# Kernel optimization log

Hardware: AMD Instinct MI355X
Metric: run time of the kernel (lower is better)

Reference implementation:

```python
import jax, jax.numpy as jnp
import numpy as np

N = 50000
E = 800000
D_IN = 64
D_OUT = 64
H = 8
R = 8  # num_relations; relation id R is reserved for self-loops
NEG_SLOPE = 0.2
EPS = 1e-10


def setup_inputs() -> dict:
    key = jax.random.key(0)
    ks = jax.random.split(key, 7)
    x = jax.random.normal(ks[0], (N, D_IN), jnp.float32)
    # xavier_uniform-like scale for W_tau, kaiming-like for query
    w_scale = (6.0 / (D_IN + D_OUT)) ** 0.5
    W_tau = jax.random.normal(ks[1], (R + 1, D_OUT, D_IN), jnp.float32) * w_scale
    query = jax.random.normal(ks[2], (R + 1, H, 2 * D_OUT // H), jnp.float32) * 0.1
    node_in = jax.random.randint(ks[3], (E,), 0, N, jnp.int32)
    node_out = jax.random.randint(ks[4], (E,), 0, N, jnp.int32)
    relation = jax.random.randint(ks[5], (E,), 0, R, jnp.int32)
    edge_weight = jax.random.uniform(ks[6], (E,), jnp.float32)
    return {"x": x, "W_tau": W_tau, "query": query, "node_in": node_in,
            "node_out": node_out, "relation": relation, "edge_weight": edge_weight}


def reference(x, W_tau, query, node_in, node_out, relation, edge_weight):
    n_node = x.shape[0]
    rp1, d_out, _ = W_tau.shape  # num_relations + 1
    n_head = query.shape[1]

    # append self-loop edges with relation id = num_relations, weight 1
    self_idx = jnp.arange(n_node, dtype=node_in.dtype)
    ni = jnp.concatenate([node_in, self_idx])            # [M]
    no = jnp.concatenate([node_out, self_idx])           # [M]
    rel = jnp.concatenate([relation, jnp.full((n_node,), rp1 - 1, dtype=relation.dtype)])
    ew = jnp.concatenate([edge_weight, jnp.ones((n_node,), edge_weight.dtype)])[:, None]  # [M,1]

    # per-relation linear transform of all nodes: [R+1, N, D_out]
    hidden = jnp.einsum('rdi,ni->rnd', W_tau, x)

    # gather endpoint features per edge (relation-specific)
    h_in = hidden[rel, ni]    # [M, D_out]
    h_out = hidden[rel, no]   # [M, D_out]
    m = h_in.shape[0]

    # interleaved stack then head split, matching torch stack(dim=-1).view
    key_feat = jnp.stack([h_in, h_out], axis=-1).reshape(m, n_head, -1)  # [M,H,2*D/H]
    w = jnp.einsum('mhd,mhd->mh', query[rel], key_feat)                  # [M,H]
    w = jax.nn.leaky_relu(w, NEG_SLOPE)

    # segment softmax (stabilized by per-node max), normalizer is scatter-MEAN (faithful)
    mx = jax.ops.segment_max(w, no, num_segments=n_node)[no]
    att = jnp.exp(w - mx) * ew                                           # [M,H]
    cnt = jax.ops.segment_sum(jnp.ones((m,), x.dtype), no, num_segments=n_node)  # [N]
    norm = (jax.ops.segment_sum(att, no, num_segments=n_node) / cnt[:, None])[no]
    att = att / (norm + EPS)

    value = h_in.reshape(m, n_head, d_out // n_head)                     # [M,H,D/H]
    msg = (att[..., None] * value).reshape(m, d_out)                     # [M,D_out]

    # aggregate: scatter-mean over destination nodes, then ReLU (combine)
    update = jax.ops.segment_sum(msg, no, num_segments=n_node) / cnt[:, None]
    return jax.nn.relu(update)
```

## Files before the change

kernel.cpp:

```cpp
#include <hip/hip_runtime.h>
#include <math.h>

#define N_NODES 50000
#define N_EDGES 800000
#define DOUT 64
#define NHEAD 8
#define RP1 9
#define NEG_SLOPE 0.2f
#define EPS_F 1e-10f
#define M_TOT (N_EDGES + N_NODES)
#define NW (RP1 * DOUT * DOUT)
#define RNG (N_NODES / 8)
#define EPB 2048
#define CHUNKS ((M_TOT + EPB - 1) / EPB)
#define BUCK 48
#define MBLK ((M_TOT + 255) / 256)
#define FILLB (CHUNKS * 8)
#define K1B ((N_NODES + 63) / 64)
#define K1PAD 784

typedef __attribute__((ext_vector_type(8))) short bf16x8;
typedef __attribute__((ext_vector_type(4))) float f32x4;

__device__ __forceinline__ unsigned short f2bf(float f) {
    unsigned int u = __float_as_uint(f);
    unsigned int r = (u + 0x7FFFu + ((u >> 16) & 1u)) >> 16;
    return (unsigned short)r;
}
__device__ __forceinline__ float bf2f(unsigned short s) {
    return __uint_as_float(((unsigned int)s) << 16);
}

__global__ __launch_bounds__(256) void kprep2(const int* __restrict__ node_in,
                                              const int* __restrict__ relation,
                                              const float* __restrict__ edge_weight,
                                              const float* __restrict__ W,
                                              int2* __restrict__ meta_by_m,
                                              unsigned short* __restrict__ Wb,
                                              int* __restrict__ cursor) {
    int m = blockIdx.x * 256 + threadIdx.x;
    if (m < NW / 4) {
        int i = m * 4;
        float4 v = *(const float4*)(W + i);
        ushort4 o; o.x = f2bf(v.x); o.y = f2bf(v.y); o.z = f2bf(v.z); o.w = f2bf(v.w);
        *(ushort4*)(Wb + i) = o;
    }
    if (m < N_NODES) cursor[m] = 0;
    if (m >= M_TOT) return;
    int ni, rl; float ew;
    if (m < N_EDGES) {
        ni = node_in[m]; rl = relation[m]; ew = edge_weight[m];
    } else {
        ni = m - N_EDGES; rl = RP1 - 1; ew = 1.0f;
    }
    int2 v; v.x = ni | (rl << 16); v.y = __float_as_int(ew);
    meta_by_m[m] = v;
}

__global__ __launch_bounds__(256) void kbig(const float* __restrict__ x,
                                            const unsigned short* __restrict__ Wb,
                                            unsigned short* __restrict__ hiddenb,
                                            const int* __restrict__ node_out,
                                            const int2* __restrict__ meta_by_m,
                                            int* __restrict__ cursor,
                                            int2* __restrict__ bucket) {
    const int t = threadIdx.x;

    if (blockIdx.x >= K1PAD) {
        const int f = blockIdx.x - K1PAD;
        const int r = f & 7;
        const int chunk = f >> 3;
        const int lo = r * RNG;
        const int hi = lo + RNG;
        int m = chunk * EPB + t;
#pragma unroll
        for (int it = 0; it < EPB / 256; it++, m += 256) {
            if (m < M_TOT) {
                int2 v = meta_by_m[m];
                int no = (m < N_EDGES) ? node_out[m] : (m - N_EDGES);
                if (no >= lo && no < hi) {
                    int pos = atomicAdd(&cursor[no], 1);
                    if (pos < BUCK) bucket[(size_t)no * BUCK + pos] = v;
                }
            }
        }
        return;
    }

    const int bx = blockIdx.x;
    if (bx >= K1B) return;
    __shared__ unsigned short st[4 * 16 * 72];
    const int wv = t >> 6, lane = t & 63;
    const int quad = lane >> 4, l16 = lane & 15;
    const int base = bx * 64 + wv * 16;

    int arow = base + l16;
    if (arow >= N_NODES) arow = N_NODES - 1;
    const float* xr = x + (size_t)arow * 64 + quad * 8;
    const float4 f0 = *(const float4*)(xr + 0);
    const float4 f1 = *(const float4*)(xr + 4);
    const float4 f2 = *(const float4*)(xr + 32);
    const float4 f3 = *(const float4*)(xr + 36);
    bf16x8 a0, a1;
    a0[0] = (short)f2bf(f0.x); a0[1] = (short)f2bf(f0.y);
    a0[2] = (short)f2bf(f0.z); a0[3] = (short)f2bf(f0.w);
    a0[4] = (short)f2bf(f1.x); a0[5] = (short)f2bf(f1.y);
    a0[6] = (short)f2bf(f1.z); a0[7] = (short)f2bf(f1.w);
    a1[0] = (short)f2bf(f2.x); a1[1] = (short)f2bf(f2.y);
    a1[2] = (short)f2bf(f2.z); a1[3] = (short)f2bf(f2.w);
    a1[4] = (short)f2bf(f3.x); a1[5] = (short)f2bf(f3.y);
    a1[6] = (short)f2bf(f3.z); a1[7] = (short)f2bf(f3.w);

    unsigned short* sw = &st[wv * 16 * 72];

    for (int r = 0; r < RP1; r++) {
        const unsigned short* Wr = Wb + r * 4096;
        f32x4 acc[4];
#pragma unroll
        for (int dt = 0; dt < 4; dt++) {
            const bf16x8 b0 = *(const bf16x8*)(Wr + (dt * 16 + l16) * 64 + quad * 8);
            const bf16x8 b1 = *(const bf16x8*)(Wr + (dt * 16 + l16) * 64 + quad * 8 + 32);
            f32x4 c = {0.f, 0.f, 0.f, 0.f};
            c = __builtin_amdgcn_mfma_f32_16x16x32_bf16(a0, b0, c, 0, 0, 0);
            c = __builtin_amdgcn_mfma_f32_16x16x32_bf16(a1, b1, c, 0, 0, 0);
            acc[dt] = c;
        }
#pragma unroll
        for (int dt = 0; dt < 4; dt++) {
#pragma unroll
            for (int v = 0; v < 4; v++) {
                sw[(quad * 4 + v) * 72 + dt * 16 + l16] = f2bf(acc[dt][v]);
            }
        }
        __threadfence_block();
#pragma unroll
        for (int q = 0; q < 2; q++) {
            int cid = q * 64 + lane;
            int row = cid >> 3;
            int ch = cid & 7;
            int n = base + row;
            if (n < N_NODES) {
                bf16x8 v = *(const bf16x8*)(sw + row * 72 + ch * 8);
                *(bf16x8*)(hiddenb + ((size_t)r * N_NODES + n) * 64 + ch * 8) = v;
            }
        }
        __threadfence_block();
    }
}

__global__ __launch_bounds__(256) void k3_fused2(const unsigned short* __restrict__ hiddenb,
                                                 const float* __restrict__ query,
                                                 const int2* __restrict__ bucket,
                                                 const int* __restrict__ deg,
                                                 float* __restrict__ out) {
    __shared__ float qe[RP1 * 64];
    __shared__ float qo[RP1 * 64];
    __shared__ float bho[4][2][72];

    const int t = threadIdx.x;
    const int wv = t >> 6, lane = t & 63;
    const int pairi = blockIdx.x * 4 + wv;
    const int nA = pairi * 2, nB = nA + 1;
    const int e_lo = lane >> 3, h = lane & 7;

    const int degAi = deg[nA], degBi = deg[nB];
    const int slot = lane & 31;
    const int nn = (lane >= 32) ? nB : nA;
    const int2 mt0 = bucket[(size_t)nn * BUCK + slot];

    const int prel = lane >> 3, ph = lane & 7;
    const bf16x8 ra = *(const bf16x8*)(hiddenb + ((size_t)(prel * N_NODES + nA)) * 64 + ph * 8);
    const bf16x8 rb = *(const bf16x8*)(hiddenb + ((size_t)(prel * N_NODES + nB)) * 64 + ph * 8);
    bf16x8 r8 = ra;
    if (lane < 16) {
        int n8 = (lane < 8) ? nA : nB;
        r8 = *(const bf16x8*)(hiddenb + ((size_t)(8 * N_NODES + n8)) * 64 + (lane & 7) * 8);
    }

    for (int q = t; q < RP1 * 64; q += 256) {
        int j = q & 7, rh = q >> 3;
        qe[q] = query[rh * 16 + 2 * j];
        qo[q] = query[rh * 16 + 2 * j + 1];
    }
    __syncthreads();

    {
        const float* qop = &qo[(prel * 8 + ph) * 8];
        float da = 0.f, db = 0.f;
#pragma unroll
        for (int j = 0; j < 8; j++) {
            da += qop[j] * bf2f((unsigned short)ra[j]);
            db += qop[j] * bf2f((unsigned short)rb[j]);
        }
        bho[wv][0][prel * 8 + ph] = da;
        bho[wv][1][prel * 8 + ph] = db;
        if (lane < 16) {
            const float* q8p = &qo[(64 + (lane & 7)) * 8];
            float d8 = 0.f;
#pragma unroll
            for (int j = 0; j < 8; j++) d8 += q8p[j] * bf2f((unsigned short)r8[j]);
            bho[wv][(lane < 8) ? 0 : 1][64 + (lane & 7)] = d8;
        }
    }
    __threadfence_block();

    const int cA = min(32, degAi);
    const int cB = min(32, degBi);
    const int npA = (cA + 7) >> 3, npB = (cB + 7) >> 3;
    const float degA = (float)degAi, degB = (float)degBi;

    float accA[8] = {0.f, 0.f, 0.f, 0.f, 0.f, 0.f, 0.f, 0.f};
    float accB[8] = {0.f, 0.f, 0.f, 0.f, 0.f, 0.f, 0.f, 0.f};
    float spA = 0.f, spB = 0.f;

    bf16x8 rA[4], rB[4];
    int relA[4], relB[4]; float ewA[4], ewB[4];
#pragma unroll
    for (int p = 0; p < 4; p++) {
        const int s = p * 8 + e_lo;
        if (p < npA) {
            int mx = __shfl(mt0.x, s);
            int my = __shfl(mt0.y, s);
            if (s >= cA) { mx = nA | ((RP1 - 1) << 16); my = 0; }
            int ni = mx & 0xffff, rl = mx >> 16;
            relA[p] = rl; ewA[p] = __int_as_float(my);
            rA[p] = *(const bf16x8*)(hiddenb + ((size_t)(rl * N_NODES + ni)) * 64 + h * 8);
        }
        if (p < npB) {
            int mx = __shfl(mt0.x, 32 + s);
            int my = __shfl(mt0.y, 32 + s);
            if (s >= cB) { mx = nB | ((RP1 - 1) << 16); my = 0; }
            int ni = mx & 0xffff, rl = mx >> 16;
            relB[p] = rl; ewB[p] = __int_as_float(my);
            rB[p] = *(const bf16x8*)(hiddenb + ((size_t)(rl * N_NODES + ni)) * 64 + h * 8);
        }
    }

#pragma unroll
    for (int p = 0; p < 4; p++) {
        if (p < npA) {
            const float* qp = &qe[(relA[p] * 8 + h) * 8];
            float hif[8];
#pragma unroll
            for (int j = 0; j < 8; j++) hif[j] = bf2f((unsigned short)rA[p][j]);
            float wp = bho[wv][0][relA[p] * 8 + h];
#pragma unroll
            for (int j = 0; j < 8; j++) wp += qp[j] * hif[j];
            wp = (wp > 0.f) ? wp : NEG_SLOPE * wp;
            float pa = __expf(wp) * ewA[p];
#pragma unroll
            for (int j = 0; j < 8; j++) accA[j] += pa * hif[j];
            spA += pa;
        }
        if (p < npB) {
            const float* qp = &qe[(relB[p] * 8 + h) * 8];
            float hif[8];
#pragma unroll
            for (int j = 0; j < 8; j++) hif[j] = bf2f((unsigned short)rB[p][j]);
            float wp = bho[wv][1][relB[p] * 8 + h];
#pragma unroll
            for (int j = 0; j < 8; j++) wp += qp[j] * hif[j];
            wp = (wp > 0.f) ? wp : NEG_SLOPE * wp;
            float pa = __expf(wp) * ewB[p];
#pragma unroll
            for (int j = 0; j < 8; j++) accB[j] += pa * hif[j];
            spB += pa;
        }
    }

    if (degAi > 32 || degBi > 32) {
        const int capA = min(degAi, BUCK), capB = min(degBi, BUCK);
#pragma unroll
        for (int p = 0; p < 2; p++) {
            const int s = 32 + p * 8 + e_lo;
            if (s < capA) {
                int2 m2 = bucket[(size_t)nA * BUCK + s];
                int ni = m2.x & 0xffff, rl = m2.x >> 16;
                float ew = __int_as_float(m2.y);
                bf16x8 r = *(const bf16x8*)(hiddenb + ((size_t)(rl * N_NODES + ni)) * 64 + h * 8);
                const float* qp = &qe[(rl * 8 + h) * 8];
                float hif[8];
#pragma unroll
                for (int j = 0; j < 8; j++) hif[j] = bf2f((unsigned short)r[j]);
                float wp = bho[wv][0][rl * 8 + h];
#pragma unroll
                for (int j = 0; j < 8; j++) wp += qp[j] * hif[j];
                wp = (wp > 0.f) ? wp : NEG_SLOPE * wp;
                float pa = __expf(wp) * ew;
#pragma unroll
                for (int j = 0; j < 8; j++) accA[j] += pa * hif[j];
                spA += pa;
            }
            if (s < capB) {
                int2 m2 = bucket[(size_t)nB * BUCK + s];
                int ni = m2.x & 0xffff, rl = m2.x >> 16;
                float ew = __int_as_float(m2.y);
                bf16x8 r = *(const bf16x8*)(hiddenb + ((size_t)(rl * N_NODES + ni)) * 64 + h * 8);
                const float* qp = &qe[(rl * 8 + h) * 8];
                float hif[8];
#pragma unroll
                for (int j = 0; j < 8; j++) hif[j] = bf2f((unsigned short)r[j]);
                float wp = bho[wv][1][rl * 8 + h];
#pragma unroll
                for (int j = 0; j < 8; j++) wp += qp[j] * hif[j];
                wp = (wp > 0.f) ? wp : NEG_SLOPE * wp;
                float pa = __expf(wp) * ew;
#pragma unroll
                for (int j = 0; j < 8; j++) accB[j] += pa * hif[j];
                spB += pa;
            }
        }
    }

#pragma unroll
    for (int j = 0; j < 8; j++) {
        accA[j] += __shfl_xor(accA[j], 8);
        accA[j] += __shfl_xor(accA[j], 16);
        accA[j] += __shfl_xor(accA[j], 32);
        accB[j] += __shfl_xor(accB[j], 8);
        accB[j] += __shfl_xor(accB[j], 16);
        accB[j] += __shfl_xor(accB[j], 32);
    }
    spA += __shfl_xor(spA, 8); spA += __shfl_xor(spA, 16); spA += __shfl_xor(spA, 32);
    spB += __shfl_xor(spB, 8); spB += __shfl_xor(spB, 16); spB += __shfl_xor(spB, 32);

    if (lane < 8) {
        const float s = 1.f / ((spA / degA + EPS_F) * degA);
        float4 o0, o1;
        o0.x = fmaxf(accA[0] * s, 0.f); o0.y = fmaxf(accA[1] * s, 0.f);
        o0.z = fmaxf(accA[2] * s, 0.f); o0.w = fmaxf(accA[3] * s, 0.f);
        o1.x = fmaxf(accA[4] * s, 0.f); o1.y = fmaxf(accA[5] * s, 0.f);
        o1.z = fmaxf(accA[6] * s, 0.f); o1.w = fmaxf(accA[7] * s, 0.f);
        float* op = out + (size_t)nA * 64 + lane * 8;
        *(float4*)(op) = o0; *(float4*)(op + 4) = o1;
    } else if (lane < 16) {
        const float s = 1.f / ((spB / degB + EPS_F) * degB);
        float4 o0, o1;
        o0.x = fmaxf(accB[0] * s, 0.f); o0.y = fmaxf(accB[1] * s, 0.f);
        o0.z = fmaxf(accB[2] * s, 0.f); o0.w = fmaxf(accB[3] * s, 0.f);
        o1.x = fmaxf(accB[4] * s, 0.f); o1.y = fmaxf(accB[5] * s, 0.f);
        o1.z = fmaxf(accB[6] * s, 0.f); o1.w = fmaxf(accB[7] * s, 0.f);
        float* op = out + (size_t)nB * 64 + (lane - 8) * 8;
        *(float4*)(op) = o0; *(float4*)(op + 4) = o1;
    }
}

extern "C" void kernel_launch(void* const* d_in, const int* in_sizes, int n_in,
                              void* d_out, int out_size, void* d_ws, size_t ws_size,
                              hipStream_t stream) {
    const float* x        = (const float*)d_in[0];
    const float* W_tau    = (const float*)d_in[1];
    const float* query    = (const float*)d_in[2];
    const int*   node_in  = (const int*)d_in[3];
    const int*   node_out = (const int*)d_in[4];
    const int*   relation = (const int*)d_in[5];
    const float* edge_w   = (const float*)d_in[6];
    float* out = (float*)d_out;

    char* ws = (char*)d_ws;
    unsigned short* hiddenb   = (unsigned short*)(ws);
    unsigned short* Wb        = (unsigned short*)(ws + 57600000);
    int2*           meta_by_m = (int2*)(ws + 57673728);
    int2*           bucket    = (int2*)(ws + 64473728);
    int*            cursor    = (int*)(ws + 83673728);

    kprep2<<<MBLK, 256, 0, stream>>>(node_in, relation, edge_w, W_tau,
                                     meta_by_m, Wb, cursor);

    kbig<<<K1PAD + FILLB, 256, 0, stream>>>(x, Wb, hiddenb, node_out, meta_by_m,
                                            cursor, bucket);

    k3_fused2<<<(N_NODES / 2 + 3) / 4, 256, 0, stream>>>(hiddenb, query, bucket,
                                                         cursor, out);
}
```

Baseline: 169.2 us.

## Replace per-node atomic buckets with block-aggregated 64-node segment binning

Edges are now binned into 64-node segments: each chunk block first counts edges per segment in shared memory, then reserves space with one global atomic per segment and scatters packed edge metadata (including the local destination id) into that segment. The aggregation kernel loads a whole segment into LDS, sorts it by local destination with a prefix scan, and processes every edge of each node instead of capping at 48. This removes the meta_by_m staging pass and most per-edge global atomics, and drops the 8-way range-filtered rescans of node_out. In exchange there is an in-block counting sort, fewer and larger blocks in the final kernel, and a segment capacity limit of 1536 edges.

Measured after the change: 168.1 us. No clear change (-0.7%).

```diff
diff --git a/kernel.cpp b/kernel.cpp
--- a/kernel.cpp
+++ b/kernel.cpp
@@ -10,14 +10,13 @@
 #define EPS_F 1e-10f
 #define M_TOT (N_EDGES + N_NODES)
 #define NW (RP1 * DOUT * DOUT)
-#define RNG (N_NODES / 8)
-#define EPB 2048
+
+#define SUBSH 6
+#define NSUB ((N_NODES + 63) >> SUBSH)
+#define SEGCAP 1536
+#define EPB 4096
 #define CHUNKS ((M_TOT + EPB - 1) / EPB)
-#define BUCK 48
-#define MBLK ((M_TOT + 255) / 256)
-#define FILLB (CHUNKS * 8)
 #define K1B ((N_NODES + 63) / 64)
-#define K1PAD 784
 
 typedef __attribute__((ext_vector_type(8))) short bf16x8;
 typedef __attribute__((ext_vector_type(4))) float f32x4;
@@ -31,13 +30,9 @@
     return __uint_as_float(((unsigned int)s) << 16);
 }
 
-__global__ __launch_bounds__(256) void kprep2(const int* __restrict__ node_in,
-                                              const int* __restrict__ relation,
-                                              const float* __restrict__ edge_weight,
-                                              const float* __restrict__ W,
-                                              int2* __restrict__ meta_by_m,
+__global__ __launch_bounds__(256) void kprep2(const float* __restrict__ W,
                                               unsigned short* __restrict__ Wb,
-                                              int* __restrict__ cursor) {
+                                              int* __restrict__ subcursor) {
     int m = blockIdx.x * 256 + threadIdx.x;
     if (m < NW / 4) {
         int i = m * 4;
@@ -45,42 +40,64 @@
         ushort4 o; o.x = f2bf(v.x); o.y = f2bf(v.y); o.z = f2bf(v.z); o.w = f2bf(v.w);
         *(ushort4*)(Wb + i) = o;
     }
-    if (m < N_NODES) cursor[m] = 0;
-    if (m >= M_TOT) return;
-    int ni, rl; float ew;
-    if (m < N_EDGES) {
-        ni = node_in[m]; rl = relation[m]; ew = edge_weight[m];
-    } else {
-        ni = m - N_EDGES; rl = RP1 - 1; ew = 1.0f;
-    }
-    int2 v; v.x = ni | (rl << 16); v.y = __float_as_int(ew);
-    meta_by_m[m] = v;
+    if (m < NSUB) subcursor[m] = 0;
 }
 
 __global__ __launch_bounds__(256) void kbig(const float* __restrict__ x,
                                             const unsigned short* __restrict__ Wb,
                                             unsigned short* __restrict__ hiddenb,
+                                            const int* __restrict__ node_in,
                                             const int* __restrict__ node_out,
-                                            const int2* __restrict__ meta_by_m,
-                                            int* __restrict__ cursor,
-                                            int2* __restrict__ bucket) {
+                                            const int* __restrict__ relation,
+                                            const float* __restrict__ edge_w,
+                                            int* __restrict__ subcursor,
+                                            int2* __restrict__ seg) {
+    __shared__ union SM {
+        unsigned short st[4 * 16 * 72];
+        struct { int cnt[NSUB]; int base[NSUB]; } f;
+    } sm;
     const int t = threadIdx.x;
 
-    if (blockIdx.x >= K1PAD) {
-        const int f = blockIdx.x - K1PAD;
-        const int r = f & 7;
-        const int chunk = f >> 3;
-        const int lo = r * RNG;
-        const int hi = lo + RNG;
-        int m = chunk * EPB + t;
-#pragma unroll
-        for (int it = 0; it < EPB / 256; it++, m += 256) {
+    if (blockIdx.x >= K1B) {
+        const int chunk = blockIdx.x - K1B;
+        const int m0 = chunk * EPB;
+        for (int s2 = t; s2 < NSUB; s2 += 256) sm.f.cnt[s2] = 0;
+        __syncthreads();
+#pragma unroll
+        for (int it = 0; it < EPB / 256; it++) {
+            int m = m0 + it * 256 + t;
             if (m < M_TOT) {
-                int2 v = meta_by_m[m];
                 int no = (m < N_EDGES) ? node_out[m] : (m - N_EDGES);
-                if (no >= lo && no < hi) {
-                    int pos = atomicAdd(&cursor[no], 1);
-                    if (pos < BUCK) bucket[(size_t)no * BUCK + pos] = v;
+                atomicAdd(&sm.f.cnt[no >> SUBSH], 1);
+            }
+        }
+        __syncthreads();
+        for (int s2 = t; s2 < NSUB; s2 += 256) {
+            int c = sm.f.cnt[s2];
+            sm.f.base[s2] = (c > 0) ? atomicAdd(&subcursor[s2], c) : 0;
+        }
+        __syncthreads();
+        for (int s2 = t; s2 < NSUB; s2 += 256) sm.f.cnt[s2] = 0;
+        __syncthreads();
+#pragma unroll
+        for (int it = 0; it < EPB / 256; it++) {
+            int m = m0 + it * 256 + t;
+            if (m < M_TOT) {
+                int no, ni, rl; float ew;
+                if (m < N_EDGES) {
+                    no = node_out[m]; ni = node_in[m];
+                    rl = relation[m]; ew = edge_w[m];
+                } else {
+                    no = m - N_EDGES; ni = no; rl = RP1 - 1; ew = 1.0f;
+                }
+                int s2 = no >> SUBSH;
+                int r = atomicAdd(&sm.f.cnt[s2], 1);
+                int pos = sm.f.base[s2] + r;
+                if (pos < SEGCAP) {
+                    int2 v;
+                    v.x = ni | (rl << 16) | ((no & 63) << 20);
+                    v.y = __float_as_int(ew);
+                    seg[(size_t)s2 * SEGCAP + pos] = v;
                 }
             }
         }
@@ -88,8 +105,6 @@
     }
 
     const int bx = blockIdx.x;
-    if (bx >= K1B) return;
-    __shared__ unsigned short st[4 * 16 * 72];
     const int wv = t >> 6, lane = t & 63;
     const int quad = lane >> 4, l16 = lane & 15;
     const int base = bx * 64 + wv * 16;
@@ -111,7 +126,7 @@
     a1[4] = (short)f2bf(f3.x); a1[5] = (short)f2bf(f3.y);
     a1[6] = (short)f2bf(f3.z); a1[7] = (short)f2bf(f3.w);
 
-    unsigned short* sw = &st[wv * 16 * 72];
+    unsigned short* sw = &sm.st[wv * 16 * 72];
 
     for (int r = 0; r < RP1; r++) {
         const unsigned short* Wr = Wb + r * 4096;
@@ -148,200 +163,185 @@
     }
 }
 
-__global__ __launch_bounds__(256) void k3_fused2(const unsigned short* __restrict__ hiddenb,
-                                                 const float* __restrict__ query,
-                                                 const int2* __restrict__ bucket,
-                                                 const int* __restrict__ deg,
-                                                 float* __restrict__ out) {
+__global__ __launch_bounds__(256) void k3_seg(const unsigned short* __restrict__ hiddenb,
+                                              const float* __restrict__ query,
+                                              const int2* __restrict__ seg,
+                                              const int* __restrict__ subcursor,
+                                              float* __restrict__ out) {
     __shared__ float qe[RP1 * 64];
     __shared__ float qo[RP1 * 64];
+    __shared__ int2  smeta[SEGCAP];
+    __shared__ unsigned short sidx[SEGCAP];
+    __shared__ int cnt[64], start[64], cnt2[64];
     __shared__ float bho[4][2][72];
 
     const int t = threadIdx.x;
-    const int wv = t >> 6, lane = t & 63;
-    const int pairi = blockIdx.x * 4 + wv;
-    const int nA = pairi * 2, nB = nA + 1;
-    const int e_lo = lane >> 3, h = lane & 7;
-
-    const int degAi = deg[nA], degBi = deg[nB];
-    const int slot = lane & 31;
-    const int nn = (lane >= 32) ? nB : nA;
-    const int2 mt0 = bucket[(size_t)nn * BUCK + slot];
-
-    const int prel = lane >> 3, ph = lane & 7;
-    const bf16x8 ra = *(const bf16x8*)(hiddenb + ((size_t)(prel * N_NODES + nA)) * 64 + ph * 8);
-    const bf16x8 rb = *(const bf16x8*)(hiddenb + ((size_t)(prel * N_NODES + nB)) * 64 + ph * 8);
-    bf16x8 r8 = ra;
-    if (lane < 16) {
-        int n8 = (lane < 8) ? nA : nB;
-        r8 = *(const bf16x8*)(hiddenb + ((size_t)(8 * N_NODES + n8)) * 64 + (lane & 7) * 8);
-    }
+    const int s = blockIdx.x;
+    const int scnt = min(subcursor[s], SEGCAP);
 
     for (int q = t; q < RP1 * 64; q += 256) {
         int j = q & 7, rh = q >> 3;
         qe[q] = query[rh * 16 + 2 * j];
         qo[q] = query[rh * 16 + 2 * j + 1];
     }
+    if (t < 64) { cnt[t] = 0; cnt2[t] = 0; }
+    for (int i = t; i < scnt; i += 256) smeta[i] = seg[(size_t)s * SEGCAP + i];
     __syncthreads();
 
-    {
-        const float* qop = &qo[(prel * 8 + ph) * 8];
-        float da = 0.f, db = 0.f;
+    for (int i = t; i < scnt; i += 256)
+        atomicAdd(&cnt[(smeta[i].x >> 20) & 63], 1);
+    __syncthreads();
+
+    if (t < 64) {
+        int v = cnt[t];
+        int sc = v;
+#pragma unroll
+        for (int d = 1; d < 64; d <<= 1) {
+            int o = __shfl_up(sc, d);
+            if (t >= d) sc += o;
+        }
+        start[t] = sc - v;
+    }
+    __syncthreads();
+
+    for (int i = t; i < scnt; i += 256) {
+        int nol = (smeta[i].x >> 20) & 63;
+        int r = atomicAdd(&cnt2[nol], 1);
+        sidx[start[nol] + r] = (unsigned short)i;
+    }
+    __syncthreads();
+
+    const int wv = t >> 6, lane = t & 63;
+    const int e_lo = lane >> 3, h = lane & 7;
+    const int prel = lane >> 3, ph = lane & 7;
+
+    for (int k = 0; k < 8; k++) {
+        const int nAl = (k * 4 + wv) * 2, nBl = nAl + 1;
+        const int nA = (s << SUBSH) + nAl, nB = nA + 1;
+        if (nA >= N_NODES) continue;
+
+        {
+            const bf16x8 ra = *(const bf16x8*)(hiddenb + ((size_t)(prel * N_NODES + nA)) * 64 + ph * 8);
+            const bf16x8 rb = *(const bf16x8*)(hiddenb + ((size_t)(prel * N_NODES + nB)) * 64 + ph * 8);
+            bf16x8 r8 = ra;
+            if (lane < 16) {
+                int n8 = (lane < 8) ? nA : nB;
+                r8 = *(const bf16x8*)(hiddenb + ((size_t)(8 * N_NODES + n8)) * 64 + (lane & 7) * 8);
+            }
+            const float* qop = &qo[(prel * 8 + ph) * 8];
+            float da = 0.f, db = 0.f;
+#pragma unroll
+            for (int j = 0; j < 8; j++) {
+                da += qop[j] * bf2f((unsigned short)ra[j]);
+                db += qop[j] * bf2f((unsigned short)rb[j]);
+            }
+            bho[wv][0][prel * 8 + ph] = da;
+            bho[wv][1][prel * 8 + ph] = db;
+            if (lane < 16) {
+                const float* q8p = &qo[(64 + (lane & 7)) * 8];
+                float d8 = 0.f;
+#pragma unroll
+                for (int j = 0; j < 8; j++) d8 += q8p[j] * bf2f((unsigned short)r8[j]);
+                bho[wv][(lane < 8) ? 0 : 1][64 + (lane & 7)] = d8;
+            }
+        }
+        __threadfence_block();
+
+        const int cA = cnt[nAl], cB = cnt[nBl];
+        const int stA = start[nAl], stB = start[nBl];
+        const float degA = (float)cA, degB = (float)cB;
+        const int cM = (cA > cB) ? cA : cB;
+
+        float accA[8] = {0.f, 0.f, 0.f, 0.f, 0.f, 0.f, 0.f, 0.f};
+        float accB[8] = {0.f, 0.f, 0.f, 0.f, 0.f, 0.f, 0.f, 0.f};
+        float spA = 0.f, spB = 0.f;
+
+        for (int j0 = 0; j0 < cM; j0 += 32) {
+            bf16x8 rA[4], rB[4];
+            int relA[4], relB[4]; float ewA[4], ewB[4];
+#pragma unroll
+            for (int p = 0; p < 4; p++) {
+                const int sa = j0 + p * 8 + e_lo;
+                if (sa < cA) {
+                    int2 mv = smeta[sidx[stA + sa]];
+                    int ni = mv.x & 0xffff;
+                    int rl = min((mv.x >> 16) & 15, RP1 - 1);
+                    relA[p] = rl; ewA[p] = __int_as_float(mv.y);
+                    rA[p] = *(const bf16x8*)(hiddenb + ((size_t)(rl * N_NODES + ni)) * 64 + h * 8);
+                }
+                if (sa < cB) {
+                    int2 mv = smeta[sidx[stB + sa]];
+                    int ni = mv.x & 0xffff;
+                    int rl = min((mv.x >> 16) & 15, RP1 - 1);
+                    relB[p] = rl; ewB[p] = __int_as_float(mv.y);
+                    rB[p] = *(const bf16x8*)(hiddenb + ((size_t)(rl * N_NODES + ni)) * 64 + h * 8);
+                }
+            }
+#pragma unroll
+            for (int p = 0; p < 4; p++) {
+                const int sa = j0 + p * 8 + e_lo;
+                if (sa < cA) {
+                    const float* qp = &qe[(relA[p] * 8 + h) * 8];
+                    float hif[8];
+#pragma unroll
+                    for (int j = 0; j < 8; j++) hif[j] = bf2f((unsigned short)rA[p][j]);
+                    float wp = bho[wv][0][relA[p] * 8 + h];
+#pragma unroll
+                    for (int j = 0; j < 8; j++) wp += qp[j] * hif[j];
+                    wp = (wp > 0.f) ? wp : NEG_SLOPE * wp;
+                    float pa = __expf(wp) * ewA[p];
+#pragma unroll
+                    for (int j = 0; j < 8; j++) accA[j] += pa * hif[j];
+                    spA += pa;
+                }
+                if (sa < cB) {
+                    const float* qp = &qe[(relB[p] * 8 + h) * 8];
+                    float hif[8];
+#pragma unroll
+                    for (int j = 0; j < 8; j++) hif[j] = bf2f((unsigned short)rB[p][j]);
+                    float wp = bho[wv][1][relB[p] * 8 + h];
+#pragma unroll
+                    for (int j = 0; j < 8; j++) wp += qp[j] * hif[j];
+                    wp = (wp > 0.f) ? wp : NEG_SLOPE * wp;
+                    float pa = __expf(wp) * ewB[p];
+#pragma unroll
+                    for (int j = 0; j < 8; j++) accB[j] += pa * hif[j];
+                    spB += pa;
+                }
+            }
+        }
+
 #pragma unroll
         for (int j = 0; j < 8; j++) {
-            da += qop[j] * bf2f((unsigned short)ra[j]);
-            db += qop[j] * bf2f((unsigned short)rb[j]);
-        }
-        bho[wv][0][prel * 8 + ph] = da;
-        bho[wv][1][prel * 8 + ph] = db;
-        if (lane < 16) {
-            const float* q8p = &qo[(64 + (lane & 7)) * 8];
-            float d8 = 0.f;
-#pragma unroll
-            for (int j = 0; j < 8; j++) d8 += q8p[j] * bf2f((unsigned short)r8[j]);
-            bho[wv][(lane < 8) ? 0 : 1][64 + (lane & 7)] = d8;
-        }
-    }
-    __threadfence_block();
-
-    const int cA = min(32, degAi);
-    const int cB = min(32, degBi);
-    const int npA = (cA + 7) >> 3, npB = (cB + 7) >> 3;
-    const float degA = (float)degAi, degB = (float)degBi;
-
-    float accA[8] = {0.f, 0.f, 0.f, 0.f, 0.f, 0.f, 0.f, 0.f};
-    float accB[8] = {0.f, 0.f, 0.f, 0.f, 0.f, 0.f, 0.f, 0.f};
-    float spA = 0.f, spB = 0.f;
-
-    bf16x8 rA[4], rB[4];
-    int relA[4], relB[4]; float ewA[4], ewB[4];
-#pragma unroll
-    for (int p = 0; p < 4; p++) {
-        const int s = p * 8 + e_lo;
-        if (p < npA) {
-            int mx = __shfl(mt0.x, s);
-            int my = __shfl(mt0.y, s);
-            if (s >= cA) { mx = nA | ((RP1 - 1) << 16); my = 0; }
-            int ni = mx & 0xffff, rl = mx >> 16;
-            relA[p] = rl; ewA[p] = __int_as_float(my);
-            rA[p] = *(const bf16x8*)(hiddenb + ((size_t)(rl * N_NODES + ni)) * 64 + h * 8);
-        }
-        if (p < npB) {
-            int mx = __shfl(mt0.x, 32 + s);
-            int my = __shfl(mt0.y, 32 + s);
-            if (s >= cB) { mx = nB | ((RP1 - 1) << 16); my = 0; }
-            int ni = mx & 0xffff, rl = mx >> 16;
-            relB[p] = rl; ewB[p] = __int_as_float(my);
-            rB[p] = *(const bf16x8*)(hiddenb + ((size_t)(rl * N_NODES + ni)) * 64 + h * 8);
-        }
-    }
-
-#pragma unroll
-    for (int p = 0; p < 4; p++) {
-        if (p < npA) {
-            const float* qp = &qe[(relA[p] * 8 + h) * 8];
-            float hif[8];
-#pragma unroll
-            for (int j = 0; j < 8; j++) hif[j] = bf2f((unsigned short)rA[p][j]);
-            float wp = bho[wv][0][relA[p] * 8 + h];
-#pragma unroll
-            for (int j = 0; j < 8; j++) wp += qp[j] * hif[j];
-            wp = (wp > 0.f) ? wp : NEG_SLOPE * wp;
-            float pa = __expf(wp) * ewA[p];
-#pragma unroll
-            for (int j = 0; j < 8; j++) accA[j] += pa * hif[j];
-            spA += pa;
-        }
-        if (p < npB) {
-            const float* qp = &qe[(relB[p] * 8 + h) * 8];
-            float hif[8];
-#pragma unroll
-            for (int j = 0; j < 8; j++) hif[j] = bf2f((unsigned short)rB[p][j]);
-            float wp = bho[wv][1][relB[p] * 8 + h];
-#pragma unroll
-            for (int j = 0; j < 8; j++) wp += qp[j] * hif[j];
-            wp = (wp > 0.f) ? wp : NEG_SLOPE * wp;
-            float pa = __expf(wp) * ewB[p];
-#pragma unroll
-            for (int j = 0; j < 8; j++) accB[j] += pa * hif[j];
-            spB += pa;
-        }
-    }
-
-    if (degAi > 32 || degBi > 32) {
-        const int capA = min(degAi, BUCK), capB = min(degBi, BUCK);
-#pragma unroll
-        for (int p = 0; p < 2; p++) {
-            const int s = 32 + p * 8 + e_lo;
-            if (s < capA) {
-                int2 m2 = bucket[(size_t)nA * BUCK + s];
-                int ni = m2.x & 0xffff, rl = m2.x >> 16;
-                float ew = __int_as_float(m2.y);
-                bf16x8 r = *(const bf16x8*)(hiddenb + ((size_t)(rl * N_NODES + ni)) * 64 + h * 8);
-                const float* qp = &qe[(rl * 8 + h) * 8];
-                float hif[8];
-#pragma unroll
-                for (int j = 0; j < 8; j++) hif[j] = bf2f((unsigned short)r[j]);
-                float wp = bho[wv][0][rl * 8 + h];
-#pragma unroll
-                for (int j = 0; j < 8; j++) wp += qp[j] * hif[j];
-                wp = (wp > 0.f) ? wp : NEG_SLOPE * wp;
-                float pa = __expf(wp) * ew;
-#pragma unroll
-                for (int j = 0; j < 8; j++) accA[j] += pa * hif[j];
-                spA += pa;
-            }
-            if (s < capB) {
-                int2 m2 = bucket[(size_t)nB * BUCK + s];
-                int ni = m2.x & 0xffff, rl = m2.x >> 16;
-                float ew = __int_as_float(m2.y);
-                bf16x8 r = *(const bf16x8*)(hiddenb + ((size_t)(rl * N_NODES + ni)) * 64 + h * 8);
-                const float* qp = &qe[(rl * 8 + h) * 8];
-                float hif[8];
-#pragma unroll
-                for (int j = 0; j < 8; j++) hif[j] = bf2f((unsigned short)r[j]);
-                float wp = bho[wv][1][rl * 8 + h];
-#pragma unroll
-                for (int j = 0; j < 8; j++) wp += qp[j] * hif[j];
-                wp = (wp > 0.f) ? wp : NEG_SLOPE * wp;
-                float pa = __expf(wp) * ew;
-#pragma unroll
-                for (int j = 0; j < 8; j++) accB[j] += pa * hif[j];
-                spB += pa;
-            }
-        }
-    }
-
-#pragma unroll
-    for (int j = 0; j < 8; j++) {
-        accA[j] += __shfl_xor(accA[j], 8);
-        accA[j] += __shfl_xor(accA[j], 16);
-        accA[j] += __shfl_xor(accA[j], 32);
-        accB[j] += __shfl_xor(accB[j], 8);
-        accB[j] += __shfl_xor(accB[j], 16);
-        accB[j] += __shfl_xor(accB[j], 32);
-    }
-    spA += __shfl_xor(spA, 8); spA += __shfl_xor(spA, 16); spA += __shfl_xor(spA, 32);
-    spB += __shfl_xor(spB, 8); spB += __shfl_xor(spB, 16); spB += __shfl_xor(spB, 32);
-
-    if (lane < 8) {
-        const float s = 1.f / ((spA / degA + EPS_F) * degA);
-        float4 o0, o1;
-        o0.x = fmaxf(accA[0] * s, 0.f); o0.y = fmaxf(accA[1] * s, 0.f);
-        o0.z = fmaxf(accA[2] * s, 0.f); o0.w = fmaxf(accA[3] * s, 0.f);
-        o1.x = fmaxf(accA[4] * s, 0.f); o1.y = fmaxf(accA[5] * s, 0.f);
-        o1.z = fmaxf(accA[6] * s, 0.f); o1.w = fmaxf(accA[7] * s, 0.f);
-        float* op = out + (size_t)nA * 64 + lane * 8;
-        *(float4*)(op) = o0; *(float4*)(op + 4) = o1;
-    } else if (lane < 16) {
-        const float s = 1.f / ((spB / degB + EPS_F) * degB);
-        float4 o0, o1;
-        o0.x = fmaxf(accB[0] * s, 0.f); o0.y = fmaxf(accB[1] * s, 0.f);
-        o0.z = fmaxf(accB[2] * s, 0.f); o0.w = fmaxf(accB[3] * s, 0.f);
-        o1.x = fmaxf(accB[4] * s, 0.f); o1.y = fmaxf(accB[5] * s, 0.f);
-        o1.z = fmaxf(accB[6] * s, 0.f); o1.w = fmaxf(accB[7] * s, 0.f);
-        float* op = out + (size_t)nB * 64 + (lane - 8) * 8;
-        *(float4*)(op) = o0; *(float4*)(op + 4) = o1;
+            accA[j] += __shfl_xor(accA[j], 8);
+            accA[j] += __shfl_xor(accA[j], 16);
+            accA[j] += __shfl_xor(accA[j], 32);
+            accB[j] += __shfl_xor(accB[j], 8);
+            accB[j] += __shfl_xor(accB[j], 16);
+            accB[j] += __shfl_xor(accB[j], 32);
+        }
+        spA += __shfl_xor(spA, 8); spA += __shfl_xor(spA, 16); spA += __shfl_xor(spA, 32);
+        spB += __shfl_xor(spB, 8); spB += __shfl_xor(spB, 16); spB += __shfl_xor(spB, 32);
+
+        if (lane < 8) {
+            const float sc = 1.f / ((spA / degA + EPS_F) * degA);
+            float4 o0, o1;
+            o0.x = fmaxf(accA[0] * sc, 0.f); o0.y = fmaxf(accA[1] * sc, 0.f);
+            o0.z = fmaxf(accA[2] * sc, 0.f); o0.w = fmaxf(accA[3] * sc, 0.f);
+            o1.x = fmaxf(accA[4] * sc, 0.f); o1.y = fmaxf(accA[5] * sc, 0.f);
+            o1.z = fmaxf(accA[6] * sc, 0.f); o1.w = fmaxf(accA[7] * sc, 0.f);
+            float* op = out + (size_t)nA * 64 + lane * 8;
+            *(float4*)(op) = o0; *(float4*)(op + 4) = o1;
+        } else if (lane < 16) {
+            const float sc = 1.f / ((spB / degB + EPS_F) * degB);
+            float4 o0, o1;
+            o0.x = fmaxf(accB[0] * sc, 0.f); o0.y = fmaxf(accB[1] * sc, 0.f);
+            o0.z = fmaxf(accB[2] * sc, 0.f); o0.w = fmaxf(accB[3] * sc, 0.f);
+            o1.x = fmaxf(accB[4] * sc, 0.f); o1.y = fmaxf(accB[5] * sc, 0.f);
+            o1.z = fmaxf(accB[6] * sc, 0.f); o1.w = fmaxf(accB[7] * sc, 0.f);
+            float* op = out + (size_t)nB * 64 + (lane - 8) * 8;
+            *(float4*)(op) = o0; *(float4*)(op + 4) = o1;
+        }
     }
 }
 
@@ -360,16 +360,13 @@
     char* ws = (char*)d_ws;
     unsigned short* hiddenb   = (unsigned short*)(ws);
     unsigned short* Wb        = (unsigned short*)(ws + 57600000);
-    int2*           meta_by_m = (int2*)(ws + 57673728);
-    int2*           bucket    = (int2*)(ws + 64473728);
-    int*            cursor    = (int*)(ws + 83673728);
-
-    kprep2<<<MBLK, 256, 0, stream>>>(node_in, relation, edge_w, W_tau,
-                                     meta_by_m, Wb, cursor);
-
-    kbig<<<K1PAD + FILLB, 256, 0, stream>>>(x, Wb, hiddenb, node_out, meta_by_m,
-                                            cursor, bucket);
-
-    k3_fused2<<<(N_NODES / 2 + 3) / 4, 256, 0, stream>>>(hiddenb, query, bucket,
-                                                         cursor, out);
-}
+    int2*           seg       = (int2*)(ws + 57673728);
+    int*            subcursor = (int*)(ws + 67282944);
+
+    kprep2<<<(NW / 4 + 255) / 256, 256, 0, stream>>>(W_tau, Wb, subcursor);
+
+    kbig<<<K1B + CHUNKS, 256, 0, stream>>>(x, Wb, hiddenb, node_in, node_out,
+                                           relation, edge_w, subcursor, seg);
+
+    k3_seg<<<NSUB, 256, 0, stream>>>(hiddenb, query, seg, subcursor, out);
+}
```
